# Performance work log

Measured on AMD Instinct MI355X. Metric: run time of the kernel, lower is better.

## Reference

```python
import jax, jax.numpy as jnp
import numpy as np

B, T, DIM, H = 4, 1024, 2048, 16
HD = DIM // H  # head_dim = 128


def _rope_tables(t, hd, theta=10000.0):
    freqs = 1.0 / (theta ** (np.arange(0, hd, 2, dtype=np.float32) / hd))  # [hd/2]
    ang = np.outer(np.arange(t, dtype=np.float32), freqs)  # [T, hd/2]
    return jnp.asarray(np.cos(ang)), jnp.asarray(np.sin(ang))


def setup_inputs() -> dict:
    key = jax.random.key(0)
    ks = jax.random.split(key, 5)
    x = jax.random.normal(ks[0], (B, T, DIM), dtype=jnp.float32)
    s = 1.0 / np.sqrt(DIM)
    wq = jax.random.normal(ks[1], (DIM, DIM), dtype=jnp.float32) * s
    wk = jax.random.normal(ks[2], (DIM, DIM), dtype=jnp.float32) * s
    wv = jax.random.normal(ks[3], (DIM, DIM), dtype=jnp.float32) * s
    wo = jax.random.normal(ks[4], (DIM, DIM), dtype=jnp.float32) * s
    freqs_cos, freqs_sin = _rope_tables(T, HD)
    return {"x": x, "freqs_cos": freqs_cos, "freqs_sin": freqs_sin,
            "wq": wq, "wk": wk, "wv": wv, "wo": wo}


def _apply_rope(t, cos, sin):
    # t: [B,T,H,HD]; cos/sin: [T,HD/2]. Adjacent feature pairs form complex numbers.
    tr = t.reshape(*t.shape[:-1], HD // 2, 2)
    te, to = tr[..., 0], tr[..., 1]
    c = cos[None, :, None, :]
    s = sin[None, :, None, :]
    oe = te * c - to * s
    oo = te * s + to * c
    return jnp.stack([oe, oo], axis=-1).reshape(t.shape)


def reference(x, freqs_cos, freqs_sin, wq, wk, wv, wo):
    # Linear layers: y = x @ W^T (torch nn.Linear convention)
    q = (x @ wq.T).reshape(B, T, H, HD)
    k = (x @ wk.T).reshape(B, T, H, HD)
    v = (x @ wv.T).reshape(B, T, H, HD)
    q = _apply_rope(q, freqs_cos, freqs_sin)
    k = _apply_rope(k, freqs_cos, freqs_sin)
    scale = 1.0 / jnp.sqrt(jnp.float32(HD))
    # non-causal SDPA (no mask in original call)
    scores = jnp.einsum('bqhd,bkhd->bhqk', q, k) * scale
    attn = jax.nn.softmax(scores, axis=-1)
    out = jnp.einsum('bhqk,bkhd->bqhd', attn, v).reshape(B, T, DIM)
    return out @ wo.T
```

## Files before the change

### kernel.cpp

```cpp
#include <hip/hip_runtime.h>
#include <stdint.h>

#define BB 4
#define TT 1024
#define DIM 2048
#define NH 16
#define HD 128
#define MR 4096
#define QKVS (3 * DIM)

typedef __attribute__((ext_vector_type(4))) float    f32x4;
typedef __attribute__((ext_vector_type(8))) uint16_t u16x8;
typedef __attribute__((ext_vector_type(4))) uint16_t u16x4;
typedef __attribute__((ext_vector_type(4))) short    s16x4;
typedef __attribute__((ext_vector_type(8))) __bf16   bf16x8;

static __device__ __forceinline__ uint16_t f2bf(float f) {
  uint32_t u = __builtin_bit_cast(uint32_t, f);
  u += 0x7fffu + ((u >> 16) & 1u);
  return (uint16_t)(u >> 16);
}
static __device__ __forceinline__ float bf2f(uint16_t b) {
  uint32_t u = ((uint32_t)b) << 16;
  return __builtin_bit_cast(float, u);
}

static __device__ __forceinline__ f32x4 mfma16(u16x8 a, u16x8 b, f32x4 c) {
  return __builtin_amdgcn_mfma_f32_16x16x32_bf16(
      __builtin_bit_cast(bf16x8, a), __builtin_bit_cast(bf16x8, b), c, 0, 0, 0);
}

static __device__ __forceinline__ void load_lds_16B(const void* g, void* l) {
  __builtin_amdgcn_global_load_lds(
      (const __attribute__((address_space(1))) void*)g,
      (__attribute__((address_space(3))) void*)l, 16, 0, 0);
}

static __device__ __forceinline__ void trpair(const uint16_t* base, int byteoff,
                                              u16x4& lo, u16x4& hi) {
  __attribute__((address_space(3))) char* ap =
      (__attribute__((address_space(3))) char*)(void*)base + byteoff;
#if defined(__has_builtin) && __has_builtin(__builtin_amdgcn_ds_read_tr16_b64_v4i16)
  s16x4 r0 = __builtin_amdgcn_ds_read_tr16_b64_v4i16(
      (__attribute__((address_space(3))) s16x4*)ap);
  s16x4 r1 = __builtin_amdgcn_ds_read_tr16_b64_v4i16(
      (__attribute__((address_space(3))) s16x4*)(ap + 128));
  lo = __builtin_bit_cast(u16x4, r0);
  hi = __builtin_bit_cast(u16x4, r1);
#else
  uint32_t a32 = (uint32_t)(uintptr_t)ap;
  asm volatile("ds_read_b64_tr_b16 %0, %2\n\t"
               "ds_read_b64_tr_b16 %1, %2 offset:128\n\t"
               "s_waitcnt lgkmcnt(0)"
               : "=&v"(lo), "=&v"(hi) : "v"(a32));
#endif
}

__global__ __launch_bounds__(256) void cast_f32_bf16(const float* __restrict__ in,
                                                     uint16_t* __restrict__ out, int n4) {
  int i = blockIdx.x * 256 + threadIdx.x;
  if (i >= n4) return;
  f32x4 v = ((const f32x4*)in)[i];
  u16x4 o;
  o[0] = f2bf(v[0]); o[1] = f2bf(v[1]); o[2] = f2bf(v[2]); o[3] = f2bf(v[3]);
  ((u16x4*)out)[i] = o;
}

__global__ __launch_bounds__(256) void cast3_f32_bf16(const float* __restrict__ s0,
                                                      const float* __restrict__ s1,
                                                      const float* __restrict__ s2,
                                                      uint16_t* __restrict__ out) {
  const int per = 4194304 / 4;
  int i = blockIdx.x * 256 + threadIdx.x;
  const float* src = (i < per) ? s0 : (i < 2 * per) ? s1 : s2;
  int j = (i < per) ? i : (i < 2 * per) ? (i - per) : (i - 2 * per);
  f32x4 v = ((const f32x4*)src)[j];
  u16x4 o;
  o[0] = f2bf(v[0]); o[1] = f2bf(v[1]); o[2] = f2bf(v[2]); o[3] = f2bf(v[3]);
  ((u16x4*)out)[i] = o;
}

template <int MODE>
__global__ __launch_bounds__(512, 1) void gemm256q(const uint16_t* __restrict__ A,
                                                   const uint16_t* __restrict__ Bt,
                                                   float* __restrict__ Cf,
                                                   uint16_t* __restrict__ Cb,
                                                   const float* __restrict__ cosT,
                                                   const float* __restrict__ sinT,
                                                   int M, int N, int K) {
  extern __shared__ __attribute__((aligned(16))) uint16_t smem[];
  const int tid  = threadIdx.x;
  const int lane = tid & 63;
  const int wave = tid >> 6;
  const int lrow = lane & 15;
  const int lgrp = lane >> 4;
  const int wr   = (wave >> 2) * 128;
  const int wc   = (wave & 3) * 64;

  const int nbx = N >> 8, nby = M >> 8;
  const int nwg = nbx * nby;
  const int wg  = ((int)blockIdx.x & 7) * (nwg >> 3) + ((int)blockIdx.x >> 3);
  const long bRow = (long)(wg / nbx) << 8;
  const long bCol = (long)(wg % nbx) << 8;

  const f32x4 fz = {0.f, 0.f, 0.f, 0.f};
  f32x4 acc[8][4];
#pragma unroll
  for (int m = 0; m < 8; ++m)
#pragma unroll
    for (int n = 0; n < 4; ++n) acc[m][n] = fz;

  auto stage = [&](int kt, int slot) {
    const long kb = (long)kt << 5;
    char* Abase = (char*)smem + slot * 32768;
    char* Bbase = Abase + 16384;
#pragma unroll
    for (int i = 0; i < 2; ++i) {
      const int L   = (i * 512 + tid) * 16;
      const int row = L >> 6;
      const int c   = ((L >> 4) & 3) ^ ((row >> 1) & 3);
      load_lds_16B(A + (bRow + row) * (long)K + kb + c * 8, Abase + L);
    }
#pragma unroll
    for (int i = 0; i < 2; ++i) {
      const int L   = (i * 512 + tid) * 16;
      const int row = L >> 6;
      const int c   = ((L >> 4) & 3) ^ ((row >> 1) & 3);
      load_lds_16B(Bt + (bCol + row) * (long)K + kb + c * 8, Bbase + L);
    }
  };

  const int NT = K >> 5;
  stage(0, 0); stage(1, 1); stage(2, 2);

  for (int t = 0; t < NT; ++t) {
    const int cur = t & 3;
    if (t < NT - 2)       asm volatile("s_waitcnt vmcnt(8)" ::: "memory");
    else if (t == NT - 2) asm volatile("s_waitcnt vmcnt(4)" ::: "memory");
    else                  asm volatile("s_waitcnt vmcnt(0)" ::: "memory");
    __builtin_amdgcn_s_barrier();
    if (t + 3 < NT) stage(t + 3, (t + 3) & 3);

    const char* Ab = (const char*)smem + cur * 32768;
    const char* Bb = Ab + 16384;
    u16x8 af[8], bf[4];
#pragma unroll
    for (int m = 0; m < 8; ++m) {
      const int row = wr + m * 16 + lrow;
      af[m] = *(const u16x8*)(Ab + row * 64 + (lgrp ^ ((row >> 1) & 3)) * 16);
    }
#pragma unroll
    for (int n = 0; n < 4; ++n) {
      const int row = wc + n * 16 + lrow;
      bf[n] = *(const u16x8*)(Bb + row * 64 + (lgrp ^ ((row >> 1) & 3)) * 16);
    }
    __builtin_amdgcn_s_setprio(1);
#pragma unroll
    for (int m = 0; m < 8; ++m)
#pragma unroll
      for (int n = 0; n < 4; ++n) acc[m][n] = mfma16(af[m], bf[n], acc[m][n]);
    __builtin_amdgcn_s_setprio(0);
  }

  const bool doRope = (MODE == 2) && (bCol < 2 * DIM);
#pragma unroll
  for (int m = 0; m < 8; ++m)
#pragma unroll
    for (int n = 0; n < 4; ++n) {
      const long grow0 = bRow + wr + m * 16 + lgrp * 4;
      const long gcol  = bCol + wc + n * 16 + lrow;
      if (doRope) {
        const int  fi  = ((int)gcol >> 1) & 63;
        const bool odd = (gcol & 1) != 0;
#pragma unroll
        for (int r = 0; r < 4; ++r) {
          const long grow = grow0 + r;
          const int  ttt  = (int)grow & (TT - 1);
          float v = acc[m][n][r];
          float p = __shfl_xor(v, 1, 64);
          float cc = cosT[ttt * 64 + fi];
          float ss = sinT[ttt * 64 + fi];
          float o  = odd ? (p * ss + v * cc) : (v * cc - p * ss);
          Cb[grow * (long)N + gcol] = f2bf(o);
        }
      } else {
#pragma unroll
        for (int r = 0; r < 4; ++r) {
          const long idx = (grow0 + r) * (long)N + gcol;
          if (MODE == 1) Cf[idx] = acc[m][n][r];
          else           Cb[idx] = f2bf(acc[m][n][r]);
        }
      }
    }
}

template <int MODE>
__global__ __launch_bounds__(256, 2) void gemm128(const uint16_t* __restrict__ A,
                                                  const uint16_t* __restrict__ Bt,
                                                  float* __restrict__ Cf,
                                                  uint16_t* __restrict__ Cb,
                                                  int M, int N, int K) {
  extern __shared__ __attribute__((aligned(16))) uint16_t smem[];
  const int tid  = threadIdx.x;
  const int lane = tid & 63;
  const int wave = tid >> 6;
  const int lrow = lane & 15;
  const int lgrp = lane >> 4;
  const int wr   = (wave >> 1) * 64;
  const int wc   = (wave & 1) * 64;

  const int nbx = N >> 7, nby = M >> 7;
  const int nwg = nbx * nby;
  const int wg  = ((int)blockIdx.x & 7) * (nwg >> 3) + ((int)blockIdx.x >> 3);
  const long bRow = (long)(wg / nbx) << 7;
  const long bCol = (long)(wg % nbx) << 7;

  const f32x4 fz = {0.f, 0.f, 0.f, 0.f};
  f32x4 acc[4][4];
#pragma unroll
  for (int m = 0; m < 4; ++m)
#pragma unroll
    for (int n = 0; n < 4; ++n) acc[m][n] = fz;

  auto stage = [&](int kt, int buf) {
    const long kb = (long)kt << 5;
    char* base = (char*)smem + buf * 16384;
#pragma unroll
    for (int i = 0; i < 2; ++i) {
      const int L   = (i * 256 + tid) * 16;
      const int row = L >> 6;
      const int c   = ((L >> 4) & 3) ^ ((row >> 1) & 3);
      load_lds_16B(A + (bRow + row) * (long)K + kb + c * 8, base + L);
    }
#pragma unroll
    for (int i = 0; i < 2; ++i) {
      const int L   = (i * 256 + tid) * 16;
      const int row = L >> 6;
      const int c   = ((L >> 4) & 3) ^ ((row >> 1) & 3);
      load_lds_16B(Bt + (bCol + row) * (long)K + kb + c * 8, base + 8192 + L);
    }
  };

  const int NT = K >> 5;
  stage(0, 0); stage(1, 1); stage(2, 2);

  for (int t = 0; t < NT; ++t) {
    const int cur = t & 3;
    if (t < NT - 2)       asm volatile("s_waitcnt vmcnt(8)" ::: "memory");
    else if (t == NT - 2) asm volatile("s_waitcnt vmcnt(4)" ::: "memory");
    else                  asm volatile("s_waitcnt vmcnt(0)" ::: "memory");
    __builtin_amdgcn_s_barrier();
    if (t + 3 < NT) stage(t + 3, (t + 3) & 3);

    const char* Ab = (const char*)smem + cur * 16384;
    const char* Bb = Ab + 8192;
    u16x8 af[4], bf[4];
#pragma unroll
    for (int m = 0; m < 4; ++m) {
      const int row = wr + m * 16 + lrow;
      af[m] = *(const u16x8*)(Ab + row * 64 + (lgrp ^ ((row >> 1) & 3)) * 16);
    }
#pragma unroll
    for (int n = 0; n < 4; ++n) {
      const int row = wc + n * 16 + lrow;
      bf[n] = *(const u16x8*)(Bb + row * 64 + (lgrp ^ ((row >> 1) & 3)) * 16);
    }
    __builtin_amdgcn_s_setprio(1);
#pragma unroll
    for (int m = 0; m < 4; ++m)
#pragma unroll
      for (int n = 0; n < 4; ++n) acc[m][n] = mfma16(af[m], bf[n], acc[m][n]);
    __builtin_amdgcn_s_setprio(0);
  }

#pragma unroll
  for (int m = 0; m < 4; ++m)
#pragma unroll
    for (int n = 0; n < 4; ++n) {
      const long grow0 = bRow + wr + m * 16 + lgrp * 4;
      const long gcol  = bCol + wc + n * 16 + lrow;
#pragma unroll
      for (int r = 0; r < 4; ++r) {
        const long idx = (grow0 + r) * (long)N + gcol;
        if (MODE == 1) Cf[idx] = acc[m][n][r];
        else           Cb[idx] = f2bf(acc[m][n][r]);
      }
    }
}

__global__ __launch_bounds__(256) void attn_fwd(const uint16_t* __restrict__ Q,
                                                const uint16_t* __restrict__ K,
                                                const uint16_t* __restrict__ V,
                                                uint16_t* __restrict__ O) {
  __shared__ __attribute__((aligned(16))) uint16_t Ks[2][64 * 128];
  __shared__ __attribute__((aligned(16))) uint16_t Vs[2][64 * 128];
  __shared__ __attribute__((aligned(16))) uint16_t Ps[4][16][72];
  const int tid  = threadIdx.x;
  const int lane = tid & 63;
  const int wave = tid >> 6;
  const int lrow = lane & 15;
  const int lgrp = lane >> 4;
  const int b  = blockIdx.x >> 4;
  const int h  = blockIdx.x & 15;
  const int qt = blockIdx.y;
  const long colBase = (long)h * HD;
  const long rs = QKVS;
  const long os = DIM;
  const long qrow0 = (long)b * TT + qt * 64 + wave * 16;

  u16x8 qf[4];
#pragma unroll
  for (int kkk = 0; kkk < 4; ++kkk)
    qf[kkk] = *(const u16x8*)(Q + (qrow0 + lrow) * rs + colBase + kkk * 32 + lgrp * 8);

  const f32x4 fz = {0.f, 0.f, 0.f, 0.f};
  f32x4 oacc[8];
#pragma unroll
  for (int nf = 0; nf < 8; ++nf) oacc[nf] = fz;
  float mst[4] = {-1e30f, -1e30f, -1e30f, -1e30f};
  float lst[4] = {0.f, 0.f, 0.f, 0.f};
  const float scale = 0.08838834764831845f;

  auto stage = [&](int kt, int buf) {
    const long krow = (long)b * TT + kt * 64;
#pragma unroll
    for (int i = 0; i < 4; ++i) {
      const int L = (i * 256 + tid) * 16;
      const int krw = L >> 8;
      const int ksc = ((L >> 4) & 15) ^ (krw & 7);
      load_lds_16B(K + (krow + krw) * rs + colBase + ksc * 8,
                   (char*)&Ks[buf][0] + L);
      const int vbl = L >> 11;
      const int vkv = ((L >> 7) & 15) * 4 + ((L >> 5) & 3);
      const int vd  = vbl * 16 + ((L >> 4) & 1) * 8;
      load_lds_16B(V + (krow + vkv) * rs + colBase + vd,
                   (char*)&Vs[buf][0] + L);
    }
  };

  stage(0, 0);

  for (int kt2 = 0; kt2 < TT / 64; ++kt2) {
    const int cur = kt2 & 1;
    if (kt2 < TT / 64 - 1) {
      stage(kt2 + 1, cur ^ 1);
      asm volatile("s_waitcnt vmcnt(8)" ::: "memory");
    } else {
      asm volatile("s_waitcnt vmcnt(0)" ::: "memory");
    }
    __builtin_amdgcn_s_barrier();

    f32x4 sacc[4];
#pragma unroll
    for (int n = 0; n < 4; ++n) sacc[n] = fz;
    __builtin_amdgcn_s_setprio(1);
#pragma unroll
    for (int kkk = 0; kkk < 4; ++kkk) {
#pragma unroll
      for (int n = 0; n < 4; ++n) {
        const int row = n * 16 + lrow;
        const int ch  = (kkk * 4 + lgrp) ^ (row & 7);
        u16x8 bfr = *(const u16x8*)((const char*)&Ks[cur][0] + row * 256 + ch * 16);
        sacc[n] = mfma16(qf[kkk], bfr, sacc[n]);
      }
    }
    __builtin_amdgcn_s_setprio(0);
#pragma unroll
    for (int n = 0; n < 4; ++n) sacc[n] *= scale;

    float rmax[4];
#pragma unroll
    for (int r = 0; r < 4; ++r)
      rmax[r] = fmaxf(fmaxf(sacc[0][r], sacc[1][r]), fmaxf(sacc[2][r], sacc[3][r]));
#pragma unroll
    for (int off = 8; off >= 1; off >>= 1)
#pragma unroll
      for (int r = 0; r < 4; ++r)
        rmax[r] = fmaxf(rmax[r], __shfl_xor(rmax[r], off, 64));

    bool need = false;
#pragma unroll
    for (int r = 0; r < 4; ++r) need = need || (rmax[r] > mst[r] + 8.0f);
    if (__any(need)) {
#pragma unroll
      for (int r = 0; r < 4; ++r) {
        float mnew  = fmaxf(mst[r], rmax[r]);
        float alpha = __expf(mst[r] - mnew);
        mst[r] = mnew;
        lst[r] *= alpha;
#pragma unroll
        for (int nf = 0; nf < 8; ++nf) oacc[nf][r] *= alpha;
      }
    }

    float rsum[4] = {0.f, 0.f, 0.f, 0.f};
#pragma unroll
    for (int n = 0; n < 4; ++n)
#pragma unroll
      for (int r = 0; r < 4; ++r) {
        float pv = __expf(sacc[n][r] - mst[r]);
        rsum[r] += pv;
        Ps[wave][lgrp * 4 + r][n * 16 + lrow] = f2bf(pv);
      }
#pragma unroll
    for (int off = 8; off >= 1; off >>= 1)
#pragma unroll
      for (int r = 0; r < 4; ++r) rsum[r] += __shfl_xor(rsum[r], off, 64);
#pragma unroll
    for (int r = 0; r < 4; ++r) lst[r] += rsum[r];

    asm volatile("s_waitcnt lgkmcnt(0)" ::: "memory");

    __builtin_amdgcn_s_setprio(1);
#pragma unroll
    for (int kk2 = 0; kk2 < 2; ++kk2) {
      u16x8 af = *(const u16x8*)&Ps[wave][lrow][kk2 * 32 + lgrp * 8];
#pragma unroll
      for (int nf = 0; nf < 8; ++nf) {
        const int vbase = nf * 2048 + kk2 * 1024 + lgrp * 256 + lrow * 8;
        u16x4 lo, hi;
        trpair(&Vs[cur][0], vbase, lo, hi);
        u16x8 bfr;
        bfr[0] = lo[0]; bfr[1] = lo[1]; bfr[2] = lo[2]; bfr[3] = lo[3];
        bfr[4] = hi[0]; bfr[5] = hi[1]; bfr[6] = hi[2]; bfr[7] = hi[3];
        oacc[nf] = mfma16(af, bfr, oacc[nf]);
      }
    }
    __builtin_amdgcn_s_setprio(0);

    __builtin_amdgcn_s_barrier();
  }

  float inv[4];
#pragma unroll
  for (int r = 0; r < 4; ++r) inv[r] = 1.0f / lst[r];
#pragma unroll
  for (int nf = 0; nf < 8; ++nf)
#pragma unroll
    for (int r = 0; r < 4; ++r)
      O[(qrow0 + lgrp * 4 + r) * os + colBase + nf * 16 + lrow] =
          f2bf(oacc[nf][r] * inv[r]);
}

extern "C" void kernel_launch(void* const* d_in, const int* in_sizes, int n_in,
                              void* d_out, int out_size, void* d_ws, size_t ws_size,
                              hipStream_t stream) {
  const float* x  = (const float*)d_in[0];
  const float* fc = (const float*)d_in[1];
  const float* fs = (const float*)d_in[2];
  const float* wq = (const float*)d_in[3];
  const float* wk = (const float*)d_in[4];
  const float* wv = (const float*)d_in[5];
  const float* wo = (const float*)d_in[6];
  float* out = (float*)d_out;

  uint16_t* w16  = (uint16_t*)d_ws;
  uint16_t* xb   = w16;
  uint16_t* wqkv = xb + 8388608;
  uint16_t* wob  = wqkv + 12582912;
  uint16_t* qkv  = wob + 4194304;
  uint16_t* ob   = qkv + 25165824;

  static int lds_ok = [] {
    (void)hipFuncSetAttribute((const void*)gemm256q<2>,
                              hipFuncAttributeMaxDynamicSharedMemorySize, 131072);
    (void)hipFuncSetAttribute((const void*)gemm128<1>,
                              hipFuncAttributeMaxDynamicSharedMemorySize, 65536);
    return 1;
  }();
  (void)lds_ok;

  cast_f32_bf16<<<8192, 256, 0, stream>>>(x, xb, 8388608 / 4);
  cast3_f32_bf16<<<3 * 4096, 256, 0, stream>>>(wq, wk, wv, wqkv);
  cast_f32_bf16<<<4096, 256, 0, stream>>>(wo, wob, 4194304 / 4);

  gemm256q<2><<<(MR / 256) * (QKVS / 256), 512, 131072, stream>>>(
      xb, wqkv, nullptr, qkv, fc, fs, MR, QKVS, DIM);

  dim3 ga(BB * NH, TT / 64);
  attn_fwd<<<ga, 256, 0, stream>>>(qkv, qkv + DIM, qkv + 2 * DIM, ob);

  gemm128<1><<<(MR / 128) * (DIM / 128), 256, 65536, stream>>>(
      ob, wob, out, nullptr, MR, DIM, DIM);
}
```

Baseline: 279.8 us.

## Double-buffer MFMA register fragments to overlap LDS reads with compute in GEMMs

Both GEMM kernels now keep two sets of register fragments and read the next k-tile's A/B fragments from LDS before issuing the MFMAs for the current tile. The loop is unrolled by two, and the wait/barrier for tile t+1 moves ahead of the current compute. The goal is to hide LDS read latency behind matrix instructions instead of stalling on it every iteration. The cost is higher VGPR pressure, which may reduce occupancy, and the loop now assumes NT is even.

```diff
diff --git a/kernel.cpp b/kernel.cpp
--- a/kernel.cpp
+++ b/kernel.cpp
@@ -131,36 +131,53 @@
   };
 
   const int NT = K >> 5;
+
+#define READF(T, FA, FB)                                                      \
+  {                                                                           \
+    const char* Ab_ = (const char*)smem + ((T) & 3) * 32768;                  \
+    const char* Bb_ = Ab_ + 16384;                                            \
+    _Pragma("unroll")                                                         \
+    for (int m = 0; m < 8; ++m) {                                             \
+      const int row = wr + m * 16 + lrow;                                     \
+      FA[m] = *(const u16x8*)(Ab_ + row * 64 + (lgrp ^ ((row >> 1) & 3)) * 16);\
+    }                                                                         \
+    _Pragma("unroll")                                                         \
+    for (int n = 0; n < 4; ++n) {                                             \
+      const int row = wc + n * 16 + lrow;                                     \
+      FB[n] = *(const u16x8*)(Bb_ + row * 64 + (lgrp ^ ((row >> 1) & 3)) * 16);\
+    }                                                                         \
+  }
+
+#define ITER(T, CA, CB, NA, NB)                                               \
+  {                                                                           \
+    if ((T) + 1 < NT) {                                                       \
+      if ((T) + 2 < NT) asm volatile("s_waitcnt vmcnt(4)" ::: "memory");      \
+      else              asm volatile("s_waitcnt vmcnt(0)" ::: "memory");      \
+      __builtin_amdgcn_s_barrier();                                           \
+      if ((T) + 3 < NT) stage((T) + 3, ((T) + 3) & 3);                        \
+      READF((T) + 1, NA, NB)                                                  \
+    }                                                                         \
+    __builtin_amdgcn_s_setprio(1);                                            \
+    _Pragma("unroll")                                                         \
+    for (int m = 0; m < 8; ++m)                                               \
+      _Pragma("unroll")                                                       \
+      for (int n = 0; n < 4; ++n) acc[m][n] = mfma16(CA[m], CB[n], acc[m][n]);\
+    __builtin_amdgcn_s_setprio(0);                                            \
+  }
+
   stage(0, 0); stage(1, 1); stage(2, 2);
-
-  for (int t = 0; t < NT; ++t) {
-    const int cur = t & 3;
-    if (t < NT - 2)       asm volatile("s_waitcnt vmcnt(8)" ::: "memory");
-    else if (t == NT - 2) asm volatile("s_waitcnt vmcnt(4)" ::: "memory");
-    else                  asm volatile("s_waitcnt vmcnt(0)" ::: "memory");
-    __builtin_amdgcn_s_barrier();
-    if (t + 3 < NT) stage(t + 3, (t + 3) & 3);
-
-    const char* Ab = (const char*)smem + cur * 32768;
-    const char* Bb = Ab + 16384;
-    u16x8 af[8], bf[4];
-#pragma unroll
-    for (int m = 0; m < 8; ++m) {
-      const int row = wr + m * 16 + lrow;
-      af[m] = *(const u16x8*)(Ab + row * 64 + (lgrp ^ ((row >> 1) & 3)) * 16);
-    }
-#pragma unroll
-    for (int n = 0; n < 4; ++n) {
-      const int row = wc + n * 16 + lrow;
-      bf[n] = *(const u16x8*)(Bb + row * 64 + (lgrp ^ ((row >> 1) & 3)) * 16);
-    }
-    __builtin_amdgcn_s_setprio(1);
-#pragma unroll
-    for (int m = 0; m < 8; ++m)
-#pragma unroll
-      for (int n = 0; n < 4; ++n) acc[m][n] = mfma16(af[m], bf[n], acc[m][n]);
-    __builtin_amdgcn_s_setprio(0);
-  }
+  asm volatile("s_waitcnt vmcnt(8)" ::: "memory");
+  __builtin_amdgcn_s_barrier();
+
+  u16x8 fa0[8], fb0[4], fa1[8], fb1[4];
+  READF(0, fa0, fb0)
+
+  for (int t = 0; t < NT; t += 2) {
+    ITER(t, fa0, fb0, fa1, fb1)
+    ITER(t + 1, fa1, fb1, fa0, fb0)
+  }
+#undef ITER
+#undef READF
 
   const bool doRope = (MODE == 2) && (bCol < 2 * DIM);
 #pragma unroll
@@ -242,36 +259,53 @@
   };
 
   const int NT = K >> 5;
+
+#define READF(T, FA, FB)                                                      \
+  {                                                                           \
+    const char* Ab_ = (const char*)smem + ((T) & 3) * 16384;                  \
+    const char* Bb_ = Ab_ + 8192;                                             \
+    _Pragma("unroll")                                                         \
+    for (int m = 0; m < 4; ++m) {                                             \
+      const int row = wr + m * 16 + lrow;                                     \
+      FA[m] = *(const u16x8*)(Ab_ + row * 64 + (lgrp ^ ((row >> 1) & 3)) * 16);\
+    }                                                                         \
+    _Pragma("unroll")                                                         \
+    for (int n = 0; n < 4; ++n) {                                             \
+      const int row = wc + n * 16 + lrow;                                     \
+      FB[n] = *(const u16x8*)(Bb_ + row * 64 + (lgrp ^ ((row >> 1) & 3)) * 16);\
+    }                                                                         \
+  }
+
+#define ITER(T, CA, CB, NA, NB)                                               \
+  {                                                                           \
+    if ((T) + 1 < NT) {                                                       \
+      if ((T) + 2 < NT) asm volatile("s_waitcnt vmcnt(4)" ::: "memory");      \
+      else              asm volatile("s_waitcnt vmcnt(0)" ::: "memory");      \
+      __builtin_amdgcn_s_barrier();                                           \
+      if ((T) + 3 < NT) stage((T) + 3, ((T) + 3) & 3);                        \
+      READF((T) + 1, NA, NB)                                                  \
+    }                                                                         \
+    __builtin_amdgcn_s_setprio(1);                                            \
+    _Pragma("unroll")                                                         \
+    for (int m = 0; m < 4; ++m)                                               \
+      _Pragma("unroll")                                                       \
+      for (int n = 0; n < 4; ++n) acc[m][n] = mfma16(CA[m], CB[n], acc[m][n]);\
+    __builtin_amdgcn_s_setprio(0);                                            \
+  }
+
   stage(0, 0); stage(1, 1); stage(2, 2);
-
-  for (int t = 0; t < NT; ++t) {
-    const int cur = t & 3;
-    if (t < NT - 2)       asm volatile("s_waitcnt vmcnt(8)" ::: "memory");
-    else if (t == NT - 2) asm volatile("s_waitcnt vmcnt(4)" ::: "memory");
-    else                  asm volatile("s_waitcnt vmcnt(0)" ::: "memory");
-    __builtin_amdgcn_s_barrier();
-    if (t + 3 < NT) stage(t + 3, (t + 3) & 3);
-
-    const char* Ab = (const char*)smem + cur * 16384;
-    const char* Bb = Ab + 8192;
-    u16x8 af[4], bf[4];
-#pragma unroll
-    for (int m = 0; m < 4; ++m) {
-      const int row = wr + m * 16 + lrow;
-      af[m] = *(const u16x8*)(Ab + row * 64 + (lgrp ^ ((row >> 1) & 3)) * 16);
-    }
-#pragma unroll
-    for (int n = 0; n < 4; ++n) {
-      const int row = wc + n * 16 + lrow;
-      bf[n] = *(const u16x8*)(Bb + row * 64 + (lgrp ^ ((row >> 1) & 3)) * 16);
-    }
-    __builtin_amdgcn_s_setprio(1);
-#pragma unroll
-    for (int m = 0; m < 4; ++m)
-#pragma unroll
-      for (int n = 0; n < 4; ++n) acc[m][n] = mfma16(af[m], bf[n], acc[m][n]);
-    __builtin_amdgcn_s_setprio(0);
-  }
+  asm volatile("s_waitcnt vmcnt(8)" ::: "memory");
+  __builtin_amdgcn_s_barrier();
+
+  u16x8 fa0[4], fb0[4], fa1[4], fb1[4];
+  READF(0, fa0, fb0)
+
+  for (int t = 0; t < NT; t += 2) {
+    ITER(t, fa0, fb0, fa1, fb1)
+    ITER(t + 1, fa1, fb1, fa0, fb0)
+  }
+#undef ITER
+#undef READF
 
 #pragma unroll
   for (int m = 0; m < 4; ++m)
```

After: 280.0 us. No clear change (+0.1%).
